# Kernel tuning notes

Measured on AMD Instinct MI355X. Metric: run time of the kernel, lower is better.

## Reference

```python
import jax, jax.numpy as jnp
import numpy as np

D_MODEL = 1024
D_HEAD = 64

def setup_inputs() -> dict:
    key = jax.random.key(0)
    ks = jax.random.split(key, 7)
    s = 1.0 / np.sqrt(D_MODEL)
    x = jax.random.normal(ks[0], (4, 4096, D_MODEL), dtype=jnp.float32)
    Wq = jax.random.uniform(ks[1], (D_MODEL, D_HEAD), jnp.float32, -s, s)
    bq = jax.random.uniform(ks[2], (D_HEAD,), jnp.float32, -s, s)
    Wk = jax.random.uniform(ks[3], (D_MODEL, D_HEAD), jnp.float32, -s, s)
    bk = jax.random.uniform(ks[4], (D_HEAD,), jnp.float32, -s, s)
    Wv = jax.random.uniform(ks[5], (D_MODEL, D_HEAD), jnp.float32, -s, s)
    bv = jax.random.uniform(ks[6], (D_HEAD,), jnp.float32, -s, s)
    return {"x": x, "Wq": Wq, "bq": bq, "Wk": Wk, "bk": bk, "Wv": Wv, "bv": bv}

def reference(x, Wq, bq, Wk, bk, Wv, bv):
    # x: [b, s, d_model] -> Q,K,V: [b, s, d_head]
    Q = jnp.einsum('bsd,dh->bsh', x, Wq) + bq
    K = jnp.einsum('bsd,dh->bsh', x, Wk) + bk
    V = jnp.einsum('bsd,dh->bsh', x, Wv) + bv
    scale = 1.0 / jnp.sqrt(jnp.asarray(D_HEAD, x.dtype))
    scores = jnp.einsum('bqh,bkh->bqk', Q, K) * scale  # [b, s, s]
    attn = jax.nn.softmax(scores, axis=-1)
    return jnp.einsum('bqk,bkh->bqh', attn, V)  # [b, s, d_head]
```

## Files before the change

kernel.cpp:

```cpp
#include <hip/hip_runtime.h>

typedef __bf16 bf16x8 __attribute__((ext_vector_type(8)));
typedef __bf16 bf16x4 __attribute__((ext_vector_type(4)));
typedef float f32x4 __attribute__((ext_vector_type(4)));
typedef unsigned short u16x8 __attribute__((ext_vector_type(8)));

union FragU { u16x8 u; bf16x8 b; };
union PackU { bf16x4 v; unsigned long long q; };

__device__ __forceinline__ unsigned short bfbits(float f) {
  __bf16 h = (__bf16)f;
  union { __bf16 h; unsigned short s; } cv; cv.h = h;
  return cv.s;
}

#define MFMA16(a, b, c) __builtin_amdgcn_mfma_f32_16x16x32_bf16((a), (b), (c), 0, 0, 0)

#define QSCALE 0.18033688011112042f

__global__ __launch_bounds__(256) void wt_kernel(
    const float* __restrict__ Wq, const float* __restrict__ Wk, const float* __restrict__ Wv,
    unsigned short* __restrict__ WF)
{
  const int m = blockIdx.x >> 5;
  const int c = blockIdx.x & 31;
  const float* W = (m == 0) ? Wq : ((m == 1) ? Wk : Wv);
  const int t = threadIdx.x >> 6;
  const int lane = threadIdx.x & 63;
  const int l15 = lane & 15;
  const int g = lane >> 4;
  unsigned short* dst = WF + ((((size_t)m * 32 + c) * 4 + t) * 64 + lane) * 8;
#pragma unroll
  for (int e = 0; e < 8; ++e)
    dst[e] = bfbits(W[(size_t)(32 * c + 8 * g + e) * 64 + (16 * t + l15)]);
}

__global__ __launch_bounds__(256, 1) void proj_kernel(
    const float* __restrict__ x, const unsigned short* __restrict__ WF,
    const float* __restrict__ bq, const float* __restrict__ bk, const float* __restrict__ bv,
    unsigned short* __restrict__ Qb, unsigned short* __restrict__ KF,
    unsigned short* __restrict__ VF)
{
  const int tid = threadIdx.x;
  const int lane = tid & 63;
  const int wid = tid >> 6;
  const int l15 = lane & 15;
  const int g = lane >> 4;
  const int row0 = blockIdx.x * 64 + wid * 16;

  f32x4 accQ[4], accK[4], accV[4];
  const f32x4 zero = {0.f, 0.f, 0.f, 0.f};
#pragma unroll
  for (int i = 0; i < 4; ++i) { accQ[i] = zero; accK[i] = zero; accV[i] = zero; }

  const float* xrow = x + (size_t)(row0 + l15) * 1024;

  f32x4 xx0[4], xx1[4];
  bf16x8 wq[2][4], wk[2][4], wv[2][4];

#define PLDX(XB, C) { xx0[XB] = *(const f32x4*)(xrow + 32 * (C) + 8 * g); \
                      xx1[XB] = *(const f32x4*)(xrow + 32 * (C) + 8 * g + 4); }
#define PLDW(WS, C) { _Pragma("unroll") for (int t = 0; t < 4; ++t) { \
    wq[WS][t] = *(const bf16x8*)(WF + ((((size_t)0 * 32 + (C)) * 4 + t) * 64 + lane) * 8); \
    wk[WS][t] = *(const bf16x8*)(WF + ((((size_t)1 * 32 + (C)) * 4 + t) * 64 + lane) * 8); \
    wv[WS][t] = *(const bf16x8*)(WF + ((((size_t)2 * 32 + (C)) * 4 + t) * 64 + lane) * 8); } }
#define PHALF(XB, WS, CXN, CWN) { \
    FragU xf; \
    _Pragma("unroll") for (int i = 0; i < 4; ++i) { \
      xf.b[i] = (__bf16)xx0[XB][i]; xf.b[4 + i] = (__bf16)xx1[XB][i]; } \
    if ((CXN) < 32) PLDX(XB, CXN); \
    _Pragma("unroll") for (int t = 0; t < 4; ++t) { \
      accQ[t] = MFMA16(xf.b, wq[WS][t], accQ[t]); \
      accK[t] = MFMA16(xf.b, wk[WS][t], accK[t]); \
      accV[t] = MFMA16(wv[WS][t], xf.b, accV[t]); } \
    if ((CWN) < 32) PLDW(WS, CWN); }

  PLDX(0, 0) PLDX(1, 1) PLDX(2, 2) PLDX(3, 3)
  PLDW(0, 0) PLDW(1, 1)

#pragma unroll 1
  for (int c = 0; c < 32; c += 4) {
    PHALF(0, 0, c + 4, c + 2)
    PHALF(1, 1, c + 5, c + 3)
    PHALF(2, 0, c + 6, c + 4)
    PHALF(3, 1, c + 7, c + 5)
  }

  const int b = blockIdx.x >> 6;
  const int kt = blockIdx.x & 63;
  const int q0 = row0 & 4095;
  unsigned short* Qbase = Qb + (size_t)b * 4096 * 64;
#pragma unroll
  for (int t = 0; t < 4; ++t) {
    const int h = 16 * t + l15;
    const float bqv = bq[h];
#pragma unroll
    for (int r = 0; r < 4; ++r)
      Qbase[(size_t)(q0 + 4 * g + r) * 64 + h] = bfbits((accQ[t][r] + bqv) * QSCALE);
  }
  unsigned short* KFb = KF + ((size_t)b * 64 + kt) * 4096;
  unsigned short* VFb = VF + ((size_t)b * 64 + kt) * 4096;
#pragma unroll
  for (int t = 0; t < 4; ++t) {
    const int h = 16 * t + l15;
    const float bkv = bk[h];
#pragma unroll
    for (int r = 0; r < 4; ++r) {
      KFb[(size_t)((wid * 2 + (t >> 1)) * 64 + (t & 1) * 32 + (l15 >> 3) * 16 + 4 * g + r) * 8 +
          (l15 & 7)] = bfbits(accK[t][r] + bkv);
      const int hv = 16 * t + 4 * g + r;
      VFb[(size_t)((t * 2 + (wid >> 1)) * 64 + (wid & 1) * 32 + (l15 >> 3) * 16 + 4 * g + r) * 8 +
          (l15 & 7)] = bfbits(accV[t][r] + bv[hv]);
    }
  }
}

__global__ __launch_bounds__(256, 2) void flash_kernel(
    const unsigned short* __restrict__ Qb, const unsigned short* __restrict__ KF,
    const unsigned short* __restrict__ VF, float* __restrict__ out)
{
  __shared__ __align__(16) unsigned char lds[36864];
  const int tid = threadIdx.x;
  const int lane = tid & 63;
  const int w = tid >> 6;
  const int l15 = lane & 15;
  const int g = lane >> 4;
  const int bid = blockIdx.x;
  const int xcd = bid & 7;
  const int b = xcd >> 1;
  const int qt = (bid >> 3) * 2 + (xcd & 1);
  const int q0 = qt * 32;

  const unsigned short* Qp = Qb + (size_t)b * 4096 * 64;
  const unsigned short* KFb = KF + (size_t)b * 262144;
  const unsigned short* VFb = VF + (size_t)b * 262144;

  const bf16x8 qfA0 = *(const bf16x8*)(Qp + (size_t)(q0 + l15) * 64 + 8 * g);
  const bf16x8 qfA1 = *(const bf16x8*)(Qp + (size_t)(q0 + l15) * 64 + 32 + 8 * g);
  const bf16x8 qfB0 = *(const bf16x8*)(Qp + (size_t)(q0 + 16 + l15) * 64 + 8 * g);
  const bf16x8 qfB1 = *(const bf16x8*)(Qp + (size_t)(q0 + 16 + l15) * 64 + 32 + 8 * g);

  f32x4 O_A[4], O_B[4];
  const f32x4 zero = {0.f, 0.f, 0.f, 0.f};
#pragma unroll
  for (int i = 0; i < 4; ++i) { O_A[i] = zero; O_B[i] = zero; }
  float mA = -INFINITY, lA = 0.f, mB = -INFINITY, lB = 0.f;
  unsigned short* PwA = (unsigned short*)lds + (w * 2 + 0) * 1152;
  unsigned short* PwB = (unsigned short*)lds + (w * 2 + 1) * 1152;

#define SM_HALF(S, mvar, lvar, OA, PW) { \
  float mt = fmaxf(fmaxf(S[0][0], S[0][1]), fmaxf(S[0][2], S[0][3])); \
  _Pragma("unroll") for (int t = 1; t < 4; ++t) \
    _Pragma("unroll") for (int r = 0; r < 4; ++r) mt = fmaxf(mt, S[t][r]); \
  mt = fmaxf(mt, __shfl_xor(mt, 16)); \
  mt = fmaxf(mt, __shfl_xor(mt, 32)); \
  if (!__all(mt <= mvar + 8.0f)) { \
    const float mnew = fmaxf(mvar, mt); \
    const float alpha = __builtin_amdgcn_exp2f(mvar - mnew); \
    mvar = mnew; lvar *= alpha; \
    _Pragma("unroll") for (int r = 0; r < 4; ++r) { \
      const float ar = __shfl(alpha, 4 * g + r); \
      OA[0][r] *= ar; OA[1][r] *= ar; OA[2][r] *= ar; OA[3][r] *= ar; } \
  } \
  float ps = 0.f; \
  _Pragma("unroll") for (int t = 0; t < 4; ++t) { \
    const float p0 = __builtin_amdgcn_exp2f(S[t][0] - mvar); \
    const float p1 = __builtin_amdgcn_exp2f(S[t][1] - mvar); \
    const float p2 = __builtin_amdgcn_exp2f(S[t][2] - mvar); \
    const float p3 = __builtin_amdgcn_exp2f(S[t][3] - mvar); \
    ps += (p0 + p1) + (p2 + p3); \
    PackU pk_; pk_.v[0] = (__bf16)p0; pk_.v[1] = (__bf16)p1; \
    pk_.v[2] = (__bf16)p2; pk_.v[3] = (__bf16)p3; \
    *(unsigned long long*)((PW) + l15 * 72 + 16 * t + 4 * g) = pk_.q; } \
  ps += __shfl_xor(ps, 16); \
  ps += __shfl_xor(ps, 32); \
  lvar += ps; }

#pragma unroll 1
  for (int kt = w; kt < 64; kt += 4) {
    const unsigned short* Kt = KFb + kt * 4096;
    const unsigned short* Vt = VFb + kt * 4096;
    bf16x8 kf[8], vf[8];
#pragma unroll
    for (int j = 0; j < 8; ++j) kf[j] = *(const bf16x8*)(Kt + (j * 64 + lane) * 8);
#pragma unroll
    for (int j = 0; j < 8; ++j) vf[j] = *(const bf16x8*)(Vt + (j * 64 + lane) * 8);
    f32x4 S_A[4], S_B[4];
#pragma unroll
    for (int t = 0; t < 4; ++t) {
      S_A[t] = zero;
      S_A[t] = MFMA16(kf[2 * t], qfA0, S_A[t]);
      S_A[t] = MFMA16(kf[2 * t + 1], qfA1, S_A[t]);
      S_B[t] = zero;
      S_B[t] = MFMA16(kf[2 * t], qfB0, S_B[t]);
      S_B[t] = MFMA16(kf[2 * t + 1], qfB1, S_B[t]);
    }
    SM_HALF(S_A, mA, lA, O_A, PwA)
    SM_HALF(S_B, mB, lB, O_B, PwB)
#pragma unroll
    for (int s = 0; s < 2; ++s) {
      const bf16x8 paA = *(const bf16x8*)(PwA + l15 * 72 + 32 * s + 8 * g);
      const bf16x8 paB = *(const bf16x8*)(PwB + l15 * 72 + 32 * s + 8 * g);
#pragma unroll
      for (int nt = 0; nt < 4; ++nt) {
        O_A[nt] = MFMA16(paA, vf[2 * nt + s], O_A[nt]);
        O_B[nt] = MFMA16(paB, vf[2 * nt + s], O_B[nt]);
      }
    }
  }

  __syncthreads();
  float* O_l = (float*)lds;
  float* mlp = (float*)(lds + 34816);
#pragma unroll
  for (int nt = 0; nt < 4; ++nt)
#pragma unroll
    for (int r = 0; r < 4; ++r) {
      O_l[((w * 2 + 0) * 16 + 4 * g + r) * 68 + 16 * nt + l15] = O_A[nt][r];
      O_l[((w * 2 + 1) * 16 + 4 * g + r) * 68 + 16 * nt + l15] = O_B[nt][r];
    }
  if (g == 0) {
    mlp[((w * 2 + 0) * 16 + l15) * 2] = mA; mlp[((w * 2 + 0) * 16 + l15) * 2 + 1] = lA;
    mlp[((w * 2 + 1) * 16 + l15) * 2] = mB; mlp[((w * 2 + 1) * 16 + l15) * 2 + 1] = lB;
  }
  __syncthreads();

  const int q = tid >> 3;
  const int h0 = (tid & 7) * 8;
  const int qh = q >> 4, qr = q & 15;
  float M = -INFINITY;
#pragma unroll
  for (int s = 0; s < 4; ++s) M = fmaxf(M, mlp[((s * 2 + qh) * 16 + qr) * 2]);
  float L = 0.f;
  f32x4 a0 = zero, a1 = zero;
#pragma unroll
  for (int s = 0; s < 4; ++s) {
    const int rowi = (s * 2 + qh) * 16 + qr;
    const float wgt = __builtin_amdgcn_exp2f(mlp[rowi * 2] - M);
    L += wgt * mlp[rowi * 2 + 1];
    const f32x4 o0 = *(const f32x4*)&O_l[rowi * 68 + h0];
    const f32x4 o1 = *(const f32x4*)&O_l[rowi * 68 + h0 + 4];
#pragma unroll
    for (int i = 0; i < 4; ++i) { a0[i] += wgt * o0[i]; a1[i] += wgt * o1[i]; }
  }
  const float inv = 1.0f / L;
  float* ob = out + ((size_t)b * 4096 + qt * 32 + q) * 64 + h0;
  f32x4 r0 = {a0[0] * inv, a0[1] * inv, a0[2] * inv, a0[3] * inv};
  f32x4 r1 = {a1[0] * inv, a1[1] * inv, a1[2] * inv, a1[3] * inv};
  *(f32x4*)ob = r0;
  *(f32x4*)(ob + 4) = r1;
}

extern "C" void kernel_launch(void* const* d_in, const int* in_sizes, int n_in,
                              void* d_out, int out_size, void* d_ws, size_t ws_size,
                              hipStream_t stream) {
  const float* x  = (const float*)d_in[0];
  const float* Wq = (const float*)d_in[1];
  const float* bq = (const float*)d_in[2];
  const float* Wk = (const float*)d_in[3];
  const float* bk = (const float*)d_in[4];
  const float* Wv = (const float*)d_in[5];
  const float* bv = (const float*)d_in[6];

  char* ws = (char*)d_ws;
  unsigned short* WF = (unsigned short*)ws;
  unsigned short* Qb = (unsigned short*)(ws + (512u << 10));
  unsigned short* KF = (unsigned short*)(ws + (512u << 10) + (2u << 20));
  unsigned short* VF = (unsigned short*)(ws + (512u << 10) + (4u << 20));
  float* out = (float*)d_out;

  hipLaunchKernelGGL(wt_kernel,    dim3(96),  dim3(256), 0, stream, Wq, Wk, Wv, WF);
  hipLaunchKernelGGL(proj_kernel,  dim3(256), dim3(256), 0, stream, x, WF, bq, bk, bv, Qb, KF, VF);
  hipLaunchKernelGGL(flash_kernel, dim3(512), dim3(256), 0, stream, Qb, KF, VF, out);
}
```

Measured before the change: 61.34 us.

## Stage projection weights through double-buffered LDS shared across waves

The projection kernel previously had every wave load the bf16 weight fragments straight from global memory into registers. Now the block loads each chunk of Q/K/V weights once, cooperatively across its waves. It writes them into a double-buffered LDS array and the MFMA loop reads its fragments from LDS, with a barrier per chunk of four k-steps. This cuts redundant global/L2 weight traffic and register pressure, but adds LDS writes and reads plus a __syncthreads per iteration.

```diff
diff --git a/kernel.cpp b/kernel.cpp
--- a/kernel.cpp
+++ b/kernel.cpp
@@ -41,6 +41,7 @@
     unsigned short* __restrict__ Qb, unsigned short* __restrict__ KF,
     unsigned short* __restrict__ VF)
 {
+  __shared__ __align__(16) unsigned short ldsW[2][3][8192];
   const int tid = threadIdx.x;
   const int lane = tid & 63;
   const int wid = tid >> 6;
@@ -56,34 +57,47 @@
   const float* xrow = x + (size_t)(row0 + l15) * 1024;
 
   f32x4 xx0[4], xx1[4];
-  bf16x8 wq[2][4], wk[2][4], wv[2][4];
+  u16x8 stW[3][4];
+
+#define WLD(W0) { _Pragma("unroll") for (int m_ = 0; m_ < 3; ++m_) \
+  _Pragma("unroll") for (int i_ = 0; i_ < 4; ++i_) \
+    stW[m_][i_] = *(const u16x8*)(WF + (size_t)(m_ * 32 + (W0) * 4) * 2048 + \
+                                  wid * 2048 + i_ * 512 + lane * 8); }
+
+#define WWR(P) { _Pragma("unroll") for (int m_ = 0; m_ < 3; ++m_) \
+  _Pragma("unroll") for (int i_ = 0; i_ < 4; ++i_) \
+    *(u16x8*)&ldsW[P][m_][wid * 2048 + i_ * 512 + lane * 8] = stW[m_][i_]; }
 
 #define PLDX(XB, C) { xx0[XB] = *(const f32x4*)(xrow + 32 * (C) + 8 * g); \
                       xx1[XB] = *(const f32x4*)(xrow + 32 * (C) + 8 * g + 4); }
-#define PLDW(WS, C) { _Pragma("unroll") for (int t = 0; t < 4; ++t) { \
-    wq[WS][t] = *(const bf16x8*)(WF + ((((size_t)0 * 32 + (C)) * 4 + t) * 64 + lane) * 8); \
-    wk[WS][t] = *(const bf16x8*)(WF + ((((size_t)1 * 32 + (C)) * 4 + t) * 64 + lane) * 8); \
-    wv[WS][t] = *(const bf16x8*)(WF + ((((size_t)2 * 32 + (C)) * 4 + t) * 64 + lane) * 8); } }
-#define PHALF(XB, WS, CXN, CWN) { \
+
+#define PHALFL(P, CW, XB, CXN) { \
     FragU xf; \
-    _Pragma("unroll") for (int i = 0; i < 4; ++i) { \
-      xf.b[i] = (__bf16)xx0[XB][i]; xf.b[4 + i] = (__bf16)xx1[XB][i]; } \
+    _Pragma("unroll") for (int i_ = 0; i_ < 4; ++i_) { \
+      xf.b[i_] = (__bf16)xx0[XB][i_]; xf.b[4 + i_] = (__bf16)xx1[XB][i_]; } \
     if ((CXN) < 32) PLDX(XB, CXN); \
     _Pragma("unroll") for (int t = 0; t < 4; ++t) { \
-      accQ[t] = MFMA16(xf.b, wq[WS][t], accQ[t]); \
-      accK[t] = MFMA16(xf.b, wk[WS][t], accK[t]); \
-      accV[t] = MFMA16(wv[WS][t], xf.b, accV[t]); } \
-    if ((CWN) < 32) PLDW(WS, CWN); }
-
+      const bf16x8 wq_ = *(const bf16x8*)&ldsW[P][0][((CW) * 4 + t) * 512 + lane * 8]; \
+      const bf16x8 wk_ = *(const bf16x8*)&ldsW[P][1][((CW) * 4 + t) * 512 + lane * 8]; \
+      const bf16x8 wv_ = *(const bf16x8*)&ldsW[P][2][((CW) * 4 + t) * 512 + lane * 8]; \
+      accQ[t] = MFMA16(xf.b, wq_, accQ[t]); \
+      accK[t] = MFMA16(xf.b, wk_, accK[t]); \
+      accV[t] = MFMA16(wv_, xf.b, accV[t]); } }
+
+  WLD(0) WWR(0) WLD(1)
   PLDX(0, 0) PLDX(1, 1) PLDX(2, 2) PLDX(3, 3)
-  PLDW(0, 0) PLDW(1, 1)
 
 #pragma unroll 1
-  for (int c = 0; c < 32; c += 4) {
-    PHALF(0, 0, c + 4, c + 2)
-    PHALF(1, 1, c + 5, c + 3)
-    PHALF(2, 0, c + 6, c + 4)
-    PHALF(3, 1, c + 7, c + 5)
+  for (int w0 = 0; w0 < 8; ++w0) {
+    const int p = w0 & 1;
+    __syncthreads();
+    if (w0 < 7) WWR(p ^ 1)
+    if (w0 < 6) WLD(w0 + 2)
+    const int c = w0 * 4;
+    PHALFL(p, 0, 0, c + 4)
+    PHALFL(p, 1, 1, c + 5)
+    PHALFL(p, 2, 2, c + 6)
+    PHALFL(p, 3, 3, c + 7)
   }
 
   const int b = blockIdx.x >> 6;
@@ -92,18 +106,18 @@
   unsigned short* Qbase = Qb + (size_t)b * 4096 * 64;
 #pragma unroll
   for (int t = 0; t < 4; ++t) {
-    const int h = 16 * t + l15;
-    const float bqv = bq[h];
+    const int hh = 16 * t + l15;
+    const float bqv = bq[hh];
 #pragma unroll
     for (int r = 0; r < 4; ++r)
-      Qbase[(size_t)(q0 + 4 * g + r) * 64 + h] = bfbits((accQ[t][r] + bqv) * QSCALE);
+      Qbase[(size_t)(q0 + 4 * g + r) * 64 + hh] = bfbits((accQ[t][r] + bqv) * QSCALE);
   }
   unsigned short* KFb = KF + ((size_t)b * 64 + kt) * 4096;
   unsigned short* VFb = VF + ((size_t)b * 64 + kt) * 4096;
 #pragma unroll
   for (int t = 0; t < 4; ++t) {
-    const int h = 16 * t + l15;
-    const float bkv = bk[h];
+    const int hh = 16 * t + l15;
+    const float bkv = bk[hh];
 #pragma unroll
     for (int r = 0; r < 4; ++r) {
       KFb[(size_t)((wid * 2 + (t >> 1)) * 64 + (t & 1) * 32 + (l15 >> 3) * 16 + 4 * g + r) * 8 +
```

Result: faster. 59.37 us (-3.2%).

## Stream x tiles into LDS via async global_load_lds and halve proj block size

Applied to the files above, without the earlier changes.

The projection kernel now fetches x through asynchronous direct global-to-LDS loads into a 4-slot XOR-swizzled ring buffer per wave, replacing per-lane register prefetch from global memory. Blocks shrink from 256 to 128 threads and the grid doubles to 512 so more CUs get work, and the K/V fragment store indexing is remapped to match. The goal is better coalesced, more deeply pipelined x reads in the memory-bound projection. It adds LDS pressure, relies on manual vmcnt waits for correctness, and each block still streams the full weight fragments from global memory.

```diff
diff --git a/kernel.cpp b/kernel.cpp
--- a/kernel.cpp
+++ b/kernel.cpp
@@ -35,81 +35,98 @@
     dst[e] = bfbits(W[(size_t)(32 * c + 8 * g + e) * 64 + (16 * t + l15)]);
 }
 
-__global__ __launch_bounds__(256, 1) void proj_kernel(
+__global__ __launch_bounds__(128, 1) void proj_kernel(
     const float* __restrict__ x, const unsigned short* __restrict__ WF,
     const float* __restrict__ bq, const float* __restrict__ bk, const float* __restrict__ bv,
     unsigned short* __restrict__ Qb, unsigned short* __restrict__ KF,
     unsigned short* __restrict__ VF)
 {
+  __shared__ __align__(16) float ldsx[2][4][2048];
   const int tid = threadIdx.x;
   const int lane = tid & 63;
   const int wid = tid >> 6;
   const int l15 = lane & 15;
   const int g = lane >> 4;
-  const int row0 = blockIdx.x * 64 + wid * 16;
+  const int h = lane >> 5;
+  const int u = lane & 31;
+  const int row0 = blockIdx.x * 32 + wid * 16;
 
   f32x4 accQ[4], accK[4], accV[4];
   const f32x4 zero = {0.f, 0.f, 0.f, 0.f};
 #pragma unroll
   for (int i = 0; i < 4; ++i) { accQ[i] = zero; accK[i] = zero; accV[i] = zero; }
 
-  const float* xrow = x + (size_t)(row0 + l15) * 1024;
-
-  f32x4 xx0[4], xx1[4];
+  const float* xw = x + (size_t)row0 * 1024;
   bf16x8 wq[2][4], wk[2][4], wv[2][4];
 
-#define PLDX(XB, C) { xx0[XB] = *(const f32x4*)(xrow + 32 * (C) + 8 * g); \
-                      xx1[XB] = *(const f32x4*)(xrow + 32 * (C) + 8 * g + 4); }
+#define XDMA(CK) { _Pragma("unroll") for (int j = 0; j < 8; ++j) { \
+    const int r_ = 2 * j + h; \
+    const float* gs_ = xw + (size_t)r_ * 1024 + (CK) * 128 + ((u ^ (r_ & 7)) * 4); \
+    __builtin_amdgcn_global_load_lds( \
+        (const __attribute__((address_space(1))) void*)gs_, \
+        (__attribute__((address_space(3))) void*)&ldsx[wid][(CK) & 3][j * 256], \
+        16, 0, 0); } }
+
 #define PLDW(WS, C) { _Pragma("unroll") for (int t = 0; t < 4; ++t) { \
     wq[WS][t] = *(const bf16x8*)(WF + ((((size_t)0 * 32 + (C)) * 4 + t) * 64 + lane) * 8); \
     wk[WS][t] = *(const bf16x8*)(WF + ((((size_t)1 * 32 + (C)) * 4 + t) * 64 + lane) * 8); \
     wv[WS][t] = *(const bf16x8*)(WF + ((((size_t)2 * 32 + (C)) * 4 + t) * 64 + lane) * 8); } }
-#define PHALF(XB, WS, CXN, CWN) { \
+
+#define PHALF2(SLOT, CL, WS, CWN) { \
+    const int ku_ = l15 & 7; \
+    const float* xb_ = &ldsx[wid][SLOT][(size_t)l15 * 128]; \
+    const f32x4 x0_ = *(const f32x4*)(xb_ + ((((CL) * 8 + 2 * g) ^ ku_) * 4)); \
+    const f32x4 x1_ = *(const f32x4*)(xb_ + ((((CL) * 8 + 2 * g + 1) ^ ku_) * 4)); \
     FragU xf; \
-    _Pragma("unroll") for (int i = 0; i < 4; ++i) { \
-      xf.b[i] = (__bf16)xx0[XB][i]; xf.b[4 + i] = (__bf16)xx1[XB][i]; } \
-    if ((CXN) < 32) PLDX(XB, CXN); \
+    _Pragma("unroll") for (int i_ = 0; i_ < 4; ++i_) { \
+      xf.b[i_] = (__bf16)x0_[i_]; xf.b[4 + i_] = (__bf16)x1_[i_]; } \
     _Pragma("unroll") for (int t = 0; t < 4; ++t) { \
       accQ[t] = MFMA16(xf.b, wq[WS][t], accQ[t]); \
       accK[t] = MFMA16(xf.b, wk[WS][t], accK[t]); \
       accV[t] = MFMA16(wv[WS][t], xf.b, accV[t]); } \
     if ((CWN) < 32) PLDW(WS, CWN); }
 
-  PLDX(0, 0) PLDX(1, 1) PLDX(2, 2) PLDX(3, 3)
+  XDMA(0) XDMA(1) XDMA(2)
   PLDW(0, 0) PLDW(1, 1)
 
 #pragma unroll 1
-  for (int c = 0; c < 32; c += 4) {
-    PHALF(0, 0, c + 4, c + 2)
-    PHALF(1, 1, c + 5, c + 3)
-    PHALF(2, 0, c + 6, c + 4)
-    PHALF(3, 1, c + 7, c + 5)
-  }
-
-  const int b = blockIdx.x >> 6;
-  const int kt = blockIdx.x & 63;
+  for (int w0 = 0; w0 < 8; ++w0) {
+    asm volatile("s_waitcnt vmcnt(16)" ::: "memory");
+    __builtin_amdgcn_sched_barrier(0);
+    if (w0 < 5) XDMA(w0 + 3)
+    const int c = w0 * 4;
+    const int sl = w0 & 3;
+    PHALF2(sl, 0, 0, c + 2)
+    PHALF2(sl, 1, 1, c + 3)
+    PHALF2(sl, 2, 0, c + 4)
+    PHALF2(sl, 3, 1, c + 5)
+  }
+
+  const int b = row0 >> 12;
   const int q0 = row0 & 4095;
+  const int kt = q0 >> 6;
+  const int r16 = (q0 >> 4) & 3;
   unsigned short* Qbase = Qb + (size_t)b * 4096 * 64;
 #pragma unroll
   for (int t = 0; t < 4; ++t) {
-    const int h = 16 * t + l15;
-    const float bqv = bq[h];
+    const int hh = 16 * t + l15;
+    const float bqv = bq[hh];
 #pragma unroll
     for (int r = 0; r < 4; ++r)
-      Qbase[(size_t)(q0 + 4 * g + r) * 64 + h] = bfbits((accQ[t][r] + bqv) * QSCALE);
+      Qbase[(size_t)(q0 + 4 * g + r) * 64 + hh] = bfbits((accQ[t][r] + bqv) * QSCALE);
   }
   unsigned short* KFb = KF + ((size_t)b * 64 + kt) * 4096;
   unsigned short* VFb = VF + ((size_t)b * 64 + kt) * 4096;
 #pragma unroll
   for (int t = 0; t < 4; ++t) {
-    const int h = 16 * t + l15;
-    const float bkv = bk[h];
+    const int hh = 16 * t + l15;
+    const float bkv = bk[hh];
 #pragma unroll
     for (int r = 0; r < 4; ++r) {
-      KFb[(size_t)((wid * 2 + (t >> 1)) * 64 + (t & 1) * 32 + (l15 >> 3) * 16 + 4 * g + r) * 8 +
+      KFb[(size_t)((r16 * 2 + (t >> 1)) * 64 + (t & 1) * 32 + (l15 >> 3) * 16 + 4 * g + r) * 8 +
           (l15 & 7)] = bfbits(accK[t][r] + bkv);
       const int hv = 16 * t + 4 * g + r;
-      VFb[(size_t)((t * 2 + (wid >> 1)) * 64 + (wid & 1) * 32 + (l15 >> 3) * 16 + 4 * g + r) * 8 +
+      VFb[(size_t)((t * 2 + (r16 >> 1)) * 64 + (r16 & 1) * 32 + (l15 >> 3) * 16 + 4 * g + r) * 8 +
           (l15 & 7)] = bfbits(accV[t][r] + bv[hv]);
     }
   }
@@ -270,6 +287,6 @@
   float* out = (float*)d_out;
 
   hipLaunchKernelGGL(wt_kernel,    dim3(96),  dim3(256), 0, stream, Wq, Wk, Wv, WF);
-  hipLaunchKernelGGL(proj_kernel,  dim3(256), dim3(256), 0, stream, x, WF, bq, bk, bv, Qb, KF, VF);
+  hipLaunchKernelGGL(proj_kernel,  dim3(512), dim3(128), 0, stream, x, WF, bq, bk, bv, Qb, KF, VF);
   hipLaunchKernelGGL(flash_kernel, dim3(512), dim3(256), 0, stream, Qb, KF, VF, out);
 }
```

Measured after the change: 61.26 us. No clear change (-0.1%).
